# Kernel tuning notes

Hardware: AMD Instinct MI355X
Metric: run time of the kernel (lower is better)

Reference implementation:

```python
import jax, jax.numpy as jnp
import numpy as np

N, M, E, D = 20000, 1024, 640000, 256


def setup_inputs() -> dict:
    key = jax.random.key(0)
    ks = jax.random.split(key, 24)
    mask = jax.random.uniform(ks[0], (N, M)) < 0.05
    init = jnp.where(mask, jax.random.uniform(ks[1], (N, M), minval=0.1, maxval=1.0), 0.0)
    inp = {
        'init': init,
        'ei_cc': jax.random.randint(ks[2], (2, E), 0, N, dtype=jnp.int32),
        'ei_cac': jax.random.randint(ks[3], (2, E), 0, N, dtype=jnp.int32),
        'ei_csc': jax.random.randint(ks[4], (2, E), 0, N, dtype=jnp.int32),
        'ea_cc': jax.random.uniform(ks[5], (E,), minval=0.1, maxval=1.0),
        'ea_cac': jax.random.uniform(ks[6], (E,), minval=0.1, maxval=1.0),
        'ea_csc': jax.random.uniform(ks[7], (E,), minval=0.1, maxval=1.0),
        # Projection MLP: Linear(1,16) -> ReLU -> Linear(16,D)
        'pW1': jax.random.normal(ks[8], (1, 16)) * 0.5,
        'pb1': jnp.zeros((16,)),
        'pW2': jax.random.normal(ks[9], (16, D)) * 0.1,
        'pb2': jnp.zeros((D,)),
        # three GCN branches, 3 layers each (all D->D)
        'W_cc': jax.random.normal(ks[10], (3, D, D)) * 0.05,
        'b_cc': jnp.zeros((3, D)),
        'W_cac': jax.random.normal(ks[11], (3, D, D)) * 0.05,
        'b_cac': jnp.zeros((3, D)),
        'W_csc': jax.random.normal(ks[12], (3, D, D)) * 0.05,
        'b_csc': jnp.zeros((3, D)),
        # meta-path attention: Linear(D, 1)
        'w_att': jax.random.normal(ks[13], (D,)) * 0.05,
        'b_att': jnp.zeros((1,)),
    }
    return inp


def projection(init, pW1, pb1, pW2, pb2):
    # torch code feeds the *indices* of nonzero columns through the MLP and
    # mean-pools per row. Vectorize: precompute MLP(j) for every column index j,
    # then masked mean.
    idx = jnp.arange(M, dtype=init.dtype)[:, None]          # [M, 1]
    h = jax.nn.relu(idx @ pW1 + pb1)                        # [M, 16]
    col_emb = h @ pW2 + pb2                                 # [M, D]
    mask = (init != 0).astype(init.dtype)                   # [N, M]
    cnt = mask.sum(axis=1)                                  # [N]
    emb = (mask @ col_emb) / jnp.maximum(cnt, 1.0)[:, None]
    return jnp.where(cnt[:, None] > 0, emb, 0.0)            # zero rows stay zero


def gcn_conv(x, edge_index, edge_weight, W, b):
    # PyG GCNConv with edge_weight: add self loops (w=1), symmetric norm.
    n = x.shape[0]
    loop = jnp.arange(n, dtype=edge_index.dtype)
    row = jnp.concatenate([edge_index[0], loop])
    col = jnp.concatenate([edge_index[1], loop])
    w = jnp.concatenate([edge_weight, jnp.ones((n,), x.dtype)])
    deg = jax.ops.segment_sum(w, col, num_segments=n)
    dinv = jnp.where(deg > 0, jax.lax.rsqrt(deg), 0.0)
    norm = dinv[row] * w * dinv[col]                        # [E+N]
    h = x @ W                                               # [N, D]
    out = jax.ops.segment_sum(norm[:, None] * h[row], col, num_segments=n)
    return out + b


def gcn_branch(x, edge_index, edge_weight, Ws, bs):
    for l in range(3):
        x = jax.nn.relu(gcn_conv(x, edge_index, edge_weight, Ws[l], bs[l]))
    return x


def reference(init, ei_cc, ei_cac, ei_csc, ea_cc, ea_cac, ea_csc,
              pW1, pb1, pW2, pb2, W_cc, b_cc, W_cac, b_cac, W_csc, b_csc,
              w_att, b_att):
    x0 = projection(init, pW1, pb1, pW2, pb2)               # [N, D]
    out_cc = gcn_branch(x0, ei_cc, ea_cc, W_cc, b_cc)
    out_cac = gcn_branch(x0, ei_cac, ea_cac, W_cac, b_cac)
    out_csc = gcn_branch(x0, ei_csc, ea_csc, W_csc, b_csc)
    emb = jnp.stack([out_cc, out_cac, out_csc], axis=0)     # [3, N, D]
    scores = jnp.einsum('pnd,d->pn', emb, w_att) + b_att[0] # [3, N]
    attn = jax.nn.softmax(scores, axis=0)                   # softmax over meta-paths
    return jnp.einsum('pn,pnd->nd', attn, emb)              # [N, D]
```

## Files before the change

### kernel.cpp

```cpp
#include <hip/hip_runtime.h>
#include <hip/hip_bf16.h>

typedef __hip_bfloat16 bf16;
typedef __bf16 v8bf __attribute__((ext_vector_type(8)));
typedef float f32x4 __attribute__((ext_vector_type(4)));
typedef unsigned int v4u __attribute__((ext_vector_type(4)));

constexpr int N = 20000, M = 1024, E = 640000, D = 256;
constexpr size_t SEGEL = (size_t)N * D;
constexpr int NCHUNK = 10000;
constexpr int NSLICE = 64;
constexpr int ESLICE = E / NSLICE;

__device__ __forceinline__ float b2f(bf16 v) { return __bfloat162float(v); }
__device__ __forceinline__ bf16 f2b(float f) { return __float2bfloat16(f); }
__device__ __forceinline__ float u2f(unsigned short u) { return __uint_as_float(((unsigned)u) << 16); }
__device__ __forceinline__ unsigned short f2u(float f) { bf16 h = __float2bfloat16(f); return *(unsigned short*)&h; }
__device__ __forceinline__ float loadf(const void* p, size_t i, int isbf) {
    return isbf ? b2f(((const bf16*)p)[i]) : ((const float*)p)[i];
}
__device__ __forceinline__ void fma8(float* acc, uint4 v, float w) {
    acc[0] = fmaf(w, u2f((unsigned short)(v.x & 0xffffu)), acc[0]);
    acc[1] = fmaf(w, u2f((unsigned short)(v.x >> 16)), acc[1]);
    acc[2] = fmaf(w, u2f((unsigned short)(v.y & 0xffffu)), acc[2]);
    acc[3] = fmaf(w, u2f((unsigned short)(v.y >> 16)), acc[3]);
    acc[4] = fmaf(w, u2f((unsigned short)(v.z & 0xffffu)), acc[4]);
    acc[5] = fmaf(w, u2f((unsigned short)(v.z >> 16)), acc[5]);
    acc[6] = fmaf(w, u2f((unsigned short)(v.w & 0xffffu)), acc[6]);
    acc[7] = fmaf(w, u2f((unsigned short)(v.w >> 16)), acc[7]);
}
__device__ __forceinline__ void add8(float* a, uint4 v) {
    a[0] += u2f((unsigned short)(v.x & 0xffffu));
    a[1] += u2f((unsigned short)(v.x >> 16));
    a[2] += u2f((unsigned short)(v.y & 0xffffu));
    a[3] += u2f((unsigned short)(v.y >> 16));
    a[4] += u2f((unsigned short)(v.z & 0xffffu));
    a[5] += u2f((unsigned short)(v.z >> 16));
    a[6] += u2f((unsigned short)(v.w & 0xffffu));
    a[7] += u2f((unsigned short)(v.w >> 16));
}
__device__ __forceinline__ unsigned pack2(float a, float b) {
    return (unsigned)f2u(a) | ((unsigned)f2u(b) << 16);
}

__global__ void detect_kernel(const void* __restrict__ ea, int* __restrict__ flag)
{
    if (threadIdx.x == 0 && blockIdx.x == 0) {
        const unsigned short* u = (const unsigned short*)ea;
        int cnt = 0;
        for (int i = 0; i < 64; i++) {
            float f = __uint_as_float(((unsigned)u[i]) << 16);
            if (f >= 0.05f && f <= 1.05f) cnt++;
        }
        *flag = (cnt >= 60) ? 1 : 0;
    }
}

__global__ __launch_bounds__(256) void prep_kernel(
    const void* __restrict__ W0, const void* __restrict__ W1, const void* __restrict__ W2,
    const void* __restrict__ pW1, const void* __restrict__ pb1,
    const void* __restrict__ pW2, const void* __restrict__ pb2,
    bf16* __restrict__ WT, bf16* __restrict__ cemb, const int* __restrict__ flag)
{
    int isbf = *flag;
    int b = blockIdx.x;
    if (b < 2304) {
        int mat = b >> 8, n = b & 255, k = threadIdx.x;
        const void* W = (mat < 3) ? W0 : (mat < 6) ? W1 : W2;
        int lm = mat - (mat < 3 ? 0 : (mat < 6 ? 3 : 6));
        WT[(size_t)mat * 65536 + n * 256 + k] =
            f2b(loadf(W, (size_t)lm * 65536 + k * 256 + n, isbf));
    } else {
        int j = b - 2304;
        int d = threadIdx.x;
        float jf = (float)j;
        float acc = loadf(pb2, d, isbf);
        #pragma unroll
        for (int k = 0; k < 16; k++) {
            float h = fmaxf(jf * loadf(pW1, k, isbf) + loadf(pb1, k, isbf), 0.0f);
            acc += h * loadf(pW2, k * 256 + d, isbf);
        }
        cemb[(size_t)j * 256 + d] = f2b(acc);
    }
}

__global__ __launch_bounds__(256) void projection_kernel(
    const void* __restrict__ init, const bf16* __restrict__ cemb,
    bf16* __restrict__ x0, const int* __restrict__ flag)
{
    __shared__ unsigned short idxs[4][1024];
    int isbf = *flag;
    int wave = threadIdx.x >> 6, lane = threadIdx.x & 63;
    int i = blockIdx.x * 4 + wave;
    unsigned long long below = (lane == 63) ? 0x7fffffffffffffffull
                                            : ((1ull << lane) - 1ull);
    int cnt = 0;
    if (isbf) {
        const unsigned short* row = (const unsigned short*)init + (size_t)i * 1024;
        for (int c0 = 0; c0 < 1024; c0 += 64) {
            bool nz = (row[c0 + lane] & 0x7fffu) != 0;
            unsigned long long m = __ballot(nz);
            if (nz) idxs[wave][cnt + __popcll(m & below)] = (unsigned short)(c0 + lane);
            cnt += __popcll(m);
        }
    } else {
        const float* row = (const float*)init + (size_t)i * 1024;
        for (int c0 = 0; c0 < 1024; c0 += 64) {
            bool nz = row[c0 + lane] != 0.0f;
            unsigned long long m = __ballot(nz);
            if (nz) idxs[wave][cnt + __popcll(m & below)] = (unsigned short)(c0 + lane);
            cnt += __popcll(m);
        }
    }
    const uint4* cr4 = (const uint4*)cemb;
    int L = lane & 31, h = lane >> 5;
    float acc[8] = {0.f, 0.f, 0.f, 0.f, 0.f, 0.f, 0.f, 0.f};
    int npair = cnt >> 1;
    int t = 0;
    for (; t + 8 <= npair; t += 8) {
        uint4 v0 = cr4[(size_t)idxs[wave][2 * (t + 0) + h] * 32 + L];
        uint4 v1 = cr4[(size_t)idxs[wave][2 * (t + 1) + h] * 32 + L];
        uint4 v2 = cr4[(size_t)idxs[wave][2 * (t + 2) + h] * 32 + L];
        uint4 v3 = cr4[(size_t)idxs[wave][2 * (t + 3) + h] * 32 + L];
        uint4 v4 = cr4[(size_t)idxs[wave][2 * (t + 4) + h] * 32 + L];
        uint4 v5 = cr4[(size_t)idxs[wave][2 * (t + 5) + h] * 32 + L];
        uint4 v6 = cr4[(size_t)idxs[wave][2 * (t + 6) + h] * 32 + L];
        uint4 v7 = cr4[(size_t)idxs[wave][2 * (t + 7) + h] * 32 + L];
        add8(acc, v0); add8(acc, v1); add8(acc, v2); add8(acc, v3);
        add8(acc, v4); add8(acc, v5); add8(acc, v6); add8(acc, v7);
    }
    for (; t < npair; t++) {
        uint4 v = cr4[(size_t)idxs[wave][2 * t + h] * 32 + L];
        add8(acc, v);
    }
    if ((cnt & 1) && h == 0) {
        uint4 v = cr4[(size_t)idxs[wave][cnt - 1] * 32 + L];
        add8(acc, v);
    }
    #pragma unroll
    for (int j = 0; j < 8; j++) acc[j] += __shfl_xor(acc[j], 32, 64);
    if (h == 0) {
        float rinv = 1.0f / fmaxf((float)cnt, 1.0f);
        v4u o;
        o.x = pack2(acc[0] * rinv, acc[1] * rinv);
        o.y = pack2(acc[2] * rinv, acc[3] * rinv);
        o.z = pack2(acc[4] * rinv, acc[5] * rinv);
        o.w = pack2(acc[6] * rinv, acc[7] * rinv);
        ((v4u*)x0)[(size_t)i * 32 + L] = o;
    }
}

__global__ __launch_bounds__(256) void countP_kernel(
    const int* __restrict__ e0, const int* __restrict__ e1, const int* __restrict__ e2,
    int* __restrict__ P)
{
    __shared__ int cur[NCHUNK];
    int b = blockIdx.x;
    int pb = b >> 7, rem = b & 127;
    int ck = rem >> 6, s = rem & 63;
    const int* ei = pb == 0 ? e0 : pb == 1 ? e1 : e2;
    int c0 = ck * NCHUNK;
    int t = threadIdx.x;
    for (int i = t; i < NCHUNK; i += 256) cur[i] = 0;
    __syncthreads();
    int ebase = s * ESLICE;
    for (int e = ebase + t; e < ebase + ESLICE; e += 256) {
        int c = ei[E + e];
        if (c >= c0 && c < c0 + NCHUNK) atomicAdd(&cur[c - c0], 1);
    }
    __syncthreads();
    int* Prow = P + ((size_t)(pb * NSLICE + s)) * N + c0;
    for (int i = t; i < NCHUNK; i += 256) Prow[i] = cur[i];
}

__global__ __launch_bounds__(256) void cnt_sum_kernel(
    const int* __restrict__ P, int* __restrict__ cnt)
{
    int id = blockIdx.x * 256 + threadIdx.x;
    if (id >= 3 * N) return;
    int pb = id / N, c = id - pb * N;
    int sum = 0;
    #pragma unroll 8
    for (int s = 0; s < NSLICE; s++)
        sum += P[((size_t)(pb * NSLICE + s)) * N + c];
    cnt[id] = sum;
}

__global__ __launch_bounds__(1024) void scan_kernel(
    const int* __restrict__ cnt, int* __restrict__ col_ptr)
{
    int pb = blockIdx.x;
    int base = pb * E;
    __shared__ int s[1024];
    int t = threadIdx.x;
    const int CH = 20;
    int i0 = t * CH;
    int sum = 0;
    for (int j = 0; j < CH; j++) { int i = i0 + j; if (i < N) sum += cnt[pb * N + i]; }
    s[t] = sum;
    __syncthreads();
    for (int off = 1; off < 1024; off <<= 1) {
        int v = (t >= off) ? s[t - off] : 0;
        __syncthreads();
        s[t] += v;
        __syncthreads();
    }
    int run = base + s[t] - sum;
    for (int j = 0; j < CH; j++) {
        int i = i0 + j;
        if (i < N) {
            col_ptr[pb * (N + 1) + i] = run;
            run += cnt[pb * N + i];
        }
    }
    if (t == 0) col_ptr[pb * (N + 1) + N] = base + E;
}

__global__ __launch_bounds__(256) void base_kernel(
    int* __restrict__ P, const int* __restrict__ col_ptr)
{
    int id = blockIdx.x * 256 + threadIdx.x;
    if (id >= 3 * N) return;
    int pb = id / N, c = id - pb * N;
    int run = col_ptr[pb * (N + 1) + c];
    for (int s = 0; s < NSLICE; s++) {
        size_t idx = ((size_t)(pb * NSLICE + s)) * N + c;
        int v = P[idx];
        P[idx] = run;
        run += v;
    }
}

__global__ __launch_bounds__(256) void fill_kernel(
    const int* __restrict__ e0, const int* __restrict__ e1, const int* __restrict__ e2,
    const void* __restrict__ a0, const void* __restrict__ a1, const void* __restrict__ a2,
    const int* __restrict__ P, int2* __restrict__ epack, const int* __restrict__ flag)
{
    __shared__ int cur[NCHUNK];
    int isbf = *flag;
    int b = blockIdx.x;
    int pb = b >> 7, rem = b & 127;
    int ck = rem >> 6, s = rem & 63;
    const int* ei = pb == 0 ? e0 : pb == 1 ? e1 : e2;
    const void* ea = pb == 0 ? a0 : pb == 1 ? a1 : a2;
    int c0 = ck * NCHUNK;
    int t = threadIdx.x;
    const int* Prow = P + ((size_t)(pb * NSLICE + s)) * N + c0;
    for (int i = t; i < NCHUNK; i += 256) cur[i] = Prow[i];
    __syncthreads();
    int ebase = s * ESLICE;
    for (int e = ebase + t; e < ebase + ESLICE; e += 256) {
        int c = ei[E + e];
        if (c >= c0 && c < c0 + NCHUNK) {
            int r = ei[e];
            float w = loadf(ea, e, isbf);
            int pos = atomicAdd(&cur[c - c0], 1);
            int2 v; v.x = r; v.y = __float_as_int(w);
            epack[pos] = v;
        }
    }
}

__global__ __launch_bounds__(256) void degsum_kernel(
    const int* __restrict__ col_ptr, const int2* __restrict__ epack,
    float* __restrict__ dinv, float* __restrict__ nloop)
{
    int wave = threadIdx.x >> 6, lane = threadIdx.x & 63;
    int pb = blockIdx.x / 5000;
    int i = (blockIdx.x - pb * 5000) * 4 + wave;
    int start = col_ptr[pb * (N + 1) + i], end = col_ptr[pb * (N + 1) + i + 1];
    float sum = 0.0f;
    for (int p = start + lane; p < end; p += 64) sum += __int_as_float(epack[p].y);
    for (int off = 1; off < 64; off <<= 1) sum += __shfl_xor(sum, off, 64);
    if (lane == 0) {
        float dg = 1.0f + sum;
        dinv[pb * N + i] = rsqrtf(dg);
        nloop[pb * N + i] = 1.0f / dg;
    }
}

__global__ __launch_bounds__(256) void snorm_sort_kernel(
    const int* __restrict__ col_ptr, const int2* __restrict__ epack,
    unsigned* __restrict__ epk2, const float* __restrict__ dinv)
{
    int wave = threadIdx.x >> 6, lane = threadIdx.x & 63;
    int pb = blockIdx.x / 5000;
    int i = (blockIdx.x - pb * 5000) * 4 + wave;
    int start = col_ptr[pb * (N + 1) + i], end = col_ptr[pb * (N + 1) + i + 1];
    float dc = dinv[pb * N + i];
    for (int base = start; base < end; base += 64) {
        int n = end - base; n = n < 64 ? n : 64;
        int key = 0x7fffffff, val = 0;
        if (lane < n) {
            int2 v = epack[base + lane];
            key = v.x;
            val = __float_as_int(dc * __int_as_float(v.y) * dinv[pb * N + v.x]);
        }
        #pragma unroll
        for (int k = 2; k <= 64; k <<= 1) {
            #pragma unroll
            for (int j = k >> 1; j > 0; j >>= 1) {
                int pk = __shfl_xor(key, j, 64);
                int pv = __shfl_xor(val, j, 64);
                bool up = (lane & k) == 0;
                bool lower = (lane & j) == 0;
                bool takeMin = (up == lower);
                bool sw = takeMin ? (pk < key) : (pk > key);
                if (sw) { key = pk; val = pv; }
            }
        }
        if (lane < n) {
            epk2[base + lane] = (unsigned)key
                              | ((unsigned)f2u(__int_as_float(val)) << 16);
        }
    }
}

__global__ __launch_bounds__(256) void aggregate_kernel(
    const bf16* __restrict__ xi0, const bf16* __restrict__ xi1, const bf16* __restrict__ xi2,
    bf16* __restrict__ yb,
    const int* __restrict__ col_ptr, const unsigned* __restrict__ epk2,
    const float* __restrict__ nloop)
{
    int wave = threadIdx.x >> 6, lane = threadIdx.x & 63;
    int pb = blockIdx.x / 5000;
    int i = (blockIdx.x - pb * 5000) * 4 + wave;
    const bf16* x = pb == 0 ? xi0 : pb == 1 ? xi1 : xi2;
    const uint4* xr = (const uint4*)x;
    int L = lane & 31, h = lane >> 5;
    int start = col_ptr[pb * (N + 1) + i], end = col_ptr[pb * (N + 1) + i + 1];
    float nl = nloop[pb * N + i];
    float acc[8];
    {
        uint4 sv = xr[(size_t)i * 32 + L];
        float self = (h == 0) ? nl : 0.0f;
        #pragma unroll
        for (int j = 0; j < 8; j++) acc[j] = 0.0f;
        fma8(acc, sv, self);
    }
    for (int base = start; base < end; base += 64) {
        int n = end - base; n = n < 64 ? n : 64;
        int ev = 0;
        if (lane < n)
            ev = (int)__builtin_nontemporal_load(epk2 + base + lane);
        int pmax = (n + 1) >> 1;
        for (int p0 = 0; p0 < pmax; p0 += 8) {
            int m = pmax - p0; m = m < 8 ? m : 8;
            uint4 v[8];
            float w[8];
            #pragma unroll
            for (int k = 0; k < 8; k++) {
                int e = 2 * (p0 + k) + h;
                int ee = __shfl(ev, e, 64);
                int rj = ee & 0xffff;
                w[k] = u2f((unsigned short)((unsigned)ee >> 16));
                if (k < m) v[k] = xr[(size_t)rj * 32 + L];
            }
            #pragma unroll
            for (int k = 0; k < 8; k++)
                if (k < m) fma8(acc, v[k], w[k]);
        }
    }
    #pragma unroll
    for (int j = 0; j < 8; j++) acc[j] += __shfl_xor(acc[j], 32, 64);
    if (h == 0) {
        v4u o;
        o.x = pack2(acc[0], acc[1]);
        o.y = pack2(acc[2], acc[3]);
        o.z = pack2(acc[4], acc[5]);
        o.w = pack2(acc[6], acc[7]);
        __builtin_nontemporal_store(o,
            (v4u*)yb + (size_t)pb * (SEGEL / 8) + (size_t)i * 32 + L);
    }
}

__global__ __launch_bounds__(256) void gemm_relu_kernel(
    const bf16* __restrict__ yb, const bf16* __restrict__ WT, int layer,
    const void* __restrict__ b0, const void* __restrict__ b1, const void* __restrict__ b2,
    bf16* __restrict__ o0, bf16* __restrict__ o1, bf16* __restrict__ o2,
    const int* __restrict__ flag)
{
    constexpr int BPL = 157;
    int isbf = *flag;
    int pl = blockIdx.x / BPL, blk = blockIdx.x - pl * BPL;
    const bf16* y = yb + (size_t)pl * SEGEL;
    const bf16* wt = WT + (size_t)(pl * 3 + layer) * 65536;
    const void* bias = pl == 0 ? b0 : pl == 1 ? b1 : b2;
    bf16* xout = pl == 0 ? o0 : pl == 1 ? o1 : o2;

    int wave = threadIdx.x >> 6, lane = threadIdx.x & 63;
    int wr = wave >> 1, wn = wave & 1;
    int m0 = blk * 128 + wr * 64;
    int n0 = wn * 128;
    int mrow = lane & 15, q = lane >> 4;

    int ar[4];
    #pragma unroll
    for (int rs = 0; rs < 4; rs++) {
        int r = m0 + rs * 16 + mrow;
        ar[rs] = r < N ? r : N - 1;
    }

    f32x4 acc[4][8] = {};
    for (int k0 = 0; k0 < 256; k0 += 32) {
        int kq = (k0 >> 3) + q;
        v8bf b[8];
        #pragma unroll
        for (int nt = 0; nt < 8; nt++)
            b[nt] = reinterpret_cast<const v8bf*>(wt + (size_t)(n0 + nt * 16 + mrow) * 256)[kq];
        #pragma unroll
        for (int rs = 0; rs < 4; rs++) {
            v8bf a = reinterpret_cast<const v8bf*>(y + (size_t)ar[rs] * 256)[kq];
            #pragma unroll
            for (int nt = 0; nt < 8; nt++)
                acc[rs][nt] = __builtin_amdgcn_mfma_f32_16x16x32_bf16(a, b[nt], acc[rs][nt], 0, 0, 0);
        }
    }
    #pragma unroll
    for (int nt = 0; nt < 8; nt++) {
        int col = n0 + nt * 16 + mrow;
        float bv = loadf(bias, (size_t)layer * 256 + col, isbf);
        #pragma unroll
        for (int rs = 0; rs < 4; rs++) {
            #pragma unroll
            for (int r = 0; r < 4; r++) {
                int row = m0 + rs * 16 + q * 4 + r;
                if (row < N)
                    xout[(size_t)row * 256 + col] = f2b(fmaxf(acc[rs][nt][r] + bv, 0.0f));
            }
        }
    }
}

__global__ __launch_bounds__(256) void attention_kernel(
    const bf16* __restrict__ e0, const bf16* __restrict__ e1, const bf16* __restrict__ e2,
    const void* __restrict__ w_att, void* __restrict__ out, int n_nodes,
    const int* __restrict__ flag)
{
    int isbf = *flag;
    int wave = threadIdx.x >> 6, lane = threadIdx.x & 63;
    int n = blockIdx.x * 4 + wave;
    if (n >= n_nodes) return;
    int d0 = lane * 4;
    float w[4], v0[4], v1[4], v2[4];
    #pragma unroll
    for (int j = 0; j < 4; j++) {
        w[j]  = loadf(w_att, d0 + j, isbf);
        v0[j] = b2f(e0[(size_t)n * 256 + d0 + j]);
        v1[j] = b2f(e1[(size_t)n * 256 + d0 + j]);
        v2[j] = b2f(e2[(size_t)n * 256 + d0 + j]);
    }
    float s0 = 0, s1 = 0, s2 = 0;
    #pragma unroll
    for (int j = 0; j < 4; j++) { s0 += v0[j] * w[j]; s1 += v1[j] * w[j]; s2 += v2[j] * w[j]; }
    for (int off = 1; off < 64; off <<= 1) {
        s0 += __shfl_xor(s0, off, 64);
        s1 += __shfl_xor(s1, off, 64);
        s2 += __shfl_xor(s2, off, 64);
    }
    float m = fmaxf(s0, fmaxf(s1, s2));
    float a0 = expf(s0 - m), a1 = expf(s1 - m), a2 = expf(s2 - m);
    float inv = 1.0f / (a0 + a1 + a2);
    a0 *= inv; a1 *= inv; a2 *= inv;
    #pragma unroll
    for (int j = 0; j < 4; j++) {
        float v = a0 * v0[j] + a1 * v1[j] + a2 * v2[j];
        if (isbf) ((bf16*)out)[(size_t)n * 256 + d0 + j] = f2b(v);
        else      ((float*)out)[(size_t)n * 256 + d0 + j] = v;
    }
}

extern "C" void kernel_launch(void* const* d_in, const int* in_sizes, int n_in,
                              void* d_out, int out_size, void* d_ws, size_t ws_size,
                              hipStream_t stream)
{
    (void)in_sizes; (void)n_in; (void)out_size; (void)ws_size;

    const void* init = d_in[0];
    const int*  ei[3] = {(const int*)d_in[1], (const int*)d_in[2], (const int*)d_in[3]};
    const void* ea[3] = {d_in[4], d_in[5], d_in[6]};
    const void* pW1 = d_in[7];
    const void* pb1 = d_in[8];
    const void* pW2 = d_in[9];
    const void* pb2 = d_in[10];
    const void* Wb[3] = {d_in[11], d_in[13], d_in[15]};
    const void* bb[3] = {d_in[12], d_in[14], d_in[16]};
    const void* w_att = d_in[17];

    char* ws = (char*)d_ws;
    size_t off = 0;
    auto carve = [&](size_t bytes) -> char* {
        off = (off + 255) & ~(size_t)255;
        char* p = ws + off; off += bytes; return p;
    };
    int*   flag  = (int*)carve(4);
    bf16*  WT    = (bf16*)carve((size_t)9 * 65536 * 2);
    bf16*  cemb  = (bf16*)carve((size_t)M * D * 2);
    bf16*  x0    = (bf16*)carve(SEGEL * 2);
    int*   cnt   = (int*)carve((size_t)3 * N * 4);
    int*   colp  = (int*)carve((size_t)3 * (N + 1) * 4);
    float* dinv  = (float*)carve((size_t)3 * N * 4);
    float* nloop = (float*)carve((size_t)3 * N * 4);
    int2*  epack = (int2*)carve((size_t)3 * E * 8);
    unsigned* epk2 = (unsigned*)carve((size_t)3 * E * 4);
    bf16*  ybuf  = (bf16*)carve((size_t)3 * SEGEL * 2);
    bf16*  bufA  = (bf16*)carve((size_t)3 * SEGEL * 2);
    bf16*  bufB  = (bf16*)carve((size_t)3 * SEGEL * 2);
    int* P = (int*)bufB;

    detect_kernel<<<1, 64, 0, stream>>>(ea[0], flag);
    prep_kernel<<<3328, 256, 0, stream>>>(Wb[0], Wb[1], Wb[2],
                                          pW1, pb1, pW2, pb2, WT, cemb, flag);
    projection_kernel<<<5000, 256, 0, stream>>>(init, cemb, x0, flag);

    countP_kernel<<<384, 256, 0, stream>>>(ei[0], ei[1], ei[2], P);
    cnt_sum_kernel<<<(3 * N + 255) / 256, 256, 0, stream>>>(P, cnt);
    scan_kernel<<<3, 1024, 0, stream>>>(cnt, colp);
    base_kernel<<<(3 * N + 255) / 256, 256, 0, stream>>>(P, colp);
    fill_kernel<<<384, 256, 0, stream>>>(ei[0], ei[1], ei[2], ea[0], ea[1], ea[2],
                                         P, epack, flag);
    degsum_kernel<<<15000, 256, 0, stream>>>(colp, epack, dinv, nloop);
    snorm_sort_kernel<<<15000, 256, 0, stream>>>(colp, epack, epk2, dinv);

    const bf16 *i0 = x0, *i1 = x0, *i2 = x0;
    bf16* dsts[3] = {bufA, bufB, bufA};
    for (int l = 0; l < 3; l++) {
        aggregate_kernel<<<15000, 256, 0, stream>>>(i0, i1, i2, ybuf, colp, epk2, nloop);
        bf16* dst = dsts[l];
        gemm_relu_kernel<<<3 * 157, 256, 0, stream>>>(ybuf, WT, l, bb[0], bb[1], bb[2],
                                                      dst, dst + SEGEL, dst + 2 * SEGEL, flag);
        i0 = dst; i1 = dst + SEGEL; i2 = dst + 2 * SEGEL;
    }
    attention_kernel<<<5000, 256, 0, stream>>>(bufA, bufA + SEGEL, bufA + 2 * SEGEL,
                                               w_att, d_out, N, flag);
}
```

Baseline: 871.1 us.

## Inline dtype detection per kernel and shrink GEMM tiles to 32 rows

Drops the single-thread detect kernel and its flag buffer; each kernel now works out the bf16/f32 input format itself with a wave ballot over the first 64 edge weights. The GEMM is retiled from 128-row blocks with a 4x8 MFMA accumulator per wave to 32-row blocks with one 16-row strip per wave, which raises the block count from 471 to 1875. The aim is to remove one launch plus the serial detection, and to improve occupancy and fill more CUs in the GEMM. In exchange each loaded B fragment is reused less, the row bounds guard is removed (20000 divides evenly by 32), and every thread repeats a small global read for detection.

Result: no change. 885.7 us (+1.7%).

```diff
diff --git a/kernel.cpp b/kernel.cpp
--- a/kernel.cpp
+++ b/kernel.cpp
@@ -18,6 +18,12 @@
 __device__ __forceinline__ unsigned short f2u(float f) { bf16 h = __float2bfloat16(f); return *(unsigned short*)&h; }
 __device__ __forceinline__ float loadf(const void* p, size_t i, int isbf) {
     return isbf ? b2f(((const bf16*)p)[i]) : ((const float*)p)[i];
+}
+__device__ __forceinline__ int detect_bf(const void* ea) {
+    int lane = threadIdx.x & 63;
+    float f = u2f(((const unsigned short*)ea)[lane]);
+    bool ok = (f >= 0.05f && f <= 1.05f);
+    return __popcll(__ballot(ok)) >= 60;
 }
 __device__ __forceinline__ void fma8(float* acc, uint4 v, float w) {
     acc[0] = fmaf(w, u2f((unsigned short)(v.x & 0xffffu)), acc[0]);
@@ -43,26 +49,13 @@
     return (unsigned)f2u(a) | ((unsigned)f2u(b) << 16);
 }
 
-__global__ void detect_kernel(const void* __restrict__ ea, int* __restrict__ flag)
-{
-    if (threadIdx.x == 0 && blockIdx.x == 0) {
-        const unsigned short* u = (const unsigned short*)ea;
-        int cnt = 0;
-        for (int i = 0; i < 64; i++) {
-            float f = __uint_as_float(((unsigned)u[i]) << 16);
-            if (f >= 0.05f && f <= 1.05f) cnt++;
-        }
-        *flag = (cnt >= 60) ? 1 : 0;
-    }
-}
-
 __global__ __launch_bounds__(256) void prep_kernel(
     const void* __restrict__ W0, const void* __restrict__ W1, const void* __restrict__ W2,
     const void* __restrict__ pW1, const void* __restrict__ pb1,
     const void* __restrict__ pW2, const void* __restrict__ pb2,
-    bf16* __restrict__ WT, bf16* __restrict__ cemb, const int* __restrict__ flag)
-{
-    int isbf = *flag;
+    bf16* __restrict__ WT, bf16* __restrict__ cemb, const void* __restrict__ ea0)
+{
+    int isbf = detect_bf(ea0);
     int b = blockIdx.x;
     if (b < 2304) {
         int mat = b >> 8, n = b & 255, k = threadIdx.x;
@@ -86,10 +79,10 @@
 
 __global__ __launch_bounds__(256) void projection_kernel(
     const void* __restrict__ init, const bf16* __restrict__ cemb,
-    bf16* __restrict__ x0, const int* __restrict__ flag)
+    bf16* __restrict__ x0, const void* __restrict__ ea0)
 {
     __shared__ unsigned short idxs[4][1024];
-    int isbf = *flag;
+    int isbf = detect_bf(ea0);
     int wave = threadIdx.x >> 6, lane = threadIdx.x & 63;
     int i = blockIdx.x * 4 + wave;
     unsigned long long below = (lane == 63) ? 0x7fffffffffffffffull
@@ -234,10 +227,10 @@
 __global__ __launch_bounds__(256) void fill_kernel(
     const int* __restrict__ e0, const int* __restrict__ e1, const int* __restrict__ e2,
     const void* __restrict__ a0, const void* __restrict__ a1, const void* __restrict__ a2,
-    const int* __restrict__ P, int2* __restrict__ epack, const int* __restrict__ flag)
+    const int* __restrict__ P, int2* __restrict__ epack)
 {
     __shared__ int cur[NCHUNK];
-    int isbf = *flag;
+    int isbf = detect_bf(a0);
     int b = blockIdx.x;
     int pb = b >> 7, rem = b & 127;
     int ck = rem >> 6, s = rem & 63;
@@ -378,42 +371,28 @@
     const bf16* __restrict__ yb, const bf16* __restrict__ WT, int layer,
     const void* __restrict__ b0, const void* __restrict__ b1, const void* __restrict__ b2,
     bf16* __restrict__ o0, bf16* __restrict__ o1, bf16* __restrict__ o2,
-    const int* __restrict__ flag)
-{
-    constexpr int BPL = 157;
-    int isbf = *flag;
-    int pl = blockIdx.x / BPL, blk = blockIdx.x - pl * BPL;
+    const void* __restrict__ ea0)
+{
+    int isbf = detect_bf(ea0);
+    int pl = blockIdx.x / 625, blk = blockIdx.x - pl * 625;
     const bf16* y = yb + (size_t)pl * SEGEL;
     const bf16* wt = WT + (size_t)(pl * 3 + layer) * 65536;
     const void* bias = pl == 0 ? b0 : pl == 1 ? b1 : b2;
     bf16* xout = pl == 0 ? o0 : pl == 1 ? o1 : o2;
 
     int wave = threadIdx.x >> 6, lane = threadIdx.x & 63;
-    int wr = wave >> 1, wn = wave & 1;
-    int m0 = blk * 128 + wr * 64;
-    int n0 = wn * 128;
+    int m0 = blk * 32 + (wave >> 1) * 16;
+    int n0 = (wave & 1) * 128;
     int mrow = lane & 15, q = lane >> 4;
 
-    int ar[4];
-    #pragma unroll
-    for (int rs = 0; rs < 4; rs++) {
-        int r = m0 + rs * 16 + mrow;
-        ar[rs] = r < N ? r : N - 1;
-    }
-
-    f32x4 acc[4][8] = {};
+    f32x4 acc[8] = {};
+    const v8bf* arow = reinterpret_cast<const v8bf*>(y + (size_t)(m0 + mrow) * 256);
     for (int k0 = 0; k0 < 256; k0 += 32) {
-        int kq = (k0 >> 3) + q;
-        v8bf b[8];
+        v8bf a = arow[(k0 >> 3) + q];
         #pragma unroll
-        for (int nt = 0; nt < 8; nt++)
-            b[nt] = reinterpret_cast<const v8bf*>(wt + (size_t)(n0 + nt * 16 + mrow) * 256)[kq];
-        #pragma unroll
-        for (int rs = 0; rs < 4; rs++) {
-            v8bf a = reinterpret_cast<const v8bf*>(y + (size_t)ar[rs] * 256)[kq];
-            #pragma unroll
-            for (int nt = 0; nt < 8; nt++)
-                acc[rs][nt] = __builtin_amdgcn_mfma_f32_16x16x32_bf16(a, b[nt], acc[rs][nt], 0, 0, 0);
+        for (int nt = 0; nt < 8; nt++) {
+            const v8bf* brow = reinterpret_cast<const v8bf*>(wt + (size_t)(n0 + nt * 16 + mrow) * 256);
+            acc[nt] = __builtin_amdgcn_mfma_f32_16x16x32_bf16(a, brow[(k0 >> 3) + q], acc[nt], 0, 0, 0);
         }
     }
     #pragma unroll
@@ -421,13 +400,9 @@
         int col = n0 + nt * 16 + mrow;
         float bv = loadf(bias, (size_t)layer * 256 + col, isbf);
         #pragma unroll
-        for (int rs = 0; rs < 4; rs++) {
-            #pragma unroll
-            for (int r = 0; r < 4; r++) {
-                int row = m0 + rs * 16 + q * 4 + r;
-                if (row < N)
-                    xout[(size_t)row * 256 + col] = f2b(fmaxf(acc[rs][nt][r] + bv, 0.0f));
-            }
+        for (int r = 0; r < 4; r++) {
+            int row = m0 + q * 4 + r;
+            xout[(size_t)row * 256 + col] = f2b(fmaxf(acc[nt][r] + bv, 0.0f));
         }
     }
 }
@@ -435,9 +410,9 @@
 __global__ __launch_bounds__(256) void attention_kernel(
     const bf16* __restrict__ e0, const bf16* __restrict__ e1, const bf16* __restrict__ e2,
     const void* __restrict__ w_att, void* __restrict__ out, int n_nodes,
-    const int* __restrict__ flag)
-{
-    int isbf = *flag;
+    const void* __restrict__ ea0)
+{
+    int isbf = detect_bf(ea0);
     int wave = threadIdx.x >> 6, lane = threadIdx.x & 63;
     int n = blockIdx.x * 4 + wave;
     if (n >= n_nodes) return;
@@ -493,7 +468,6 @@
         off = (off + 255) & ~(size_t)255;
         char* p = ws + off; off += bytes; return p;
     };
-    int*   flag  = (int*)carve(4);
     bf16*  WT    = (bf16*)carve((size_t)9 * 65536 * 2);
     bf16*  cemb  = (bf16*)carve((size_t)M * D * 2);
     bf16*  x0    = (bf16*)carve(SEGEL * 2);
@@ -508,17 +482,16 @@
     bf16*  bufB  = (bf16*)carve((size_t)3 * SEGEL * 2);
     int* P = (int*)bufB;
 
-    detect_kernel<<<1, 64, 0, stream>>>(ea[0], flag);
     prep_kernel<<<3328, 256, 0, stream>>>(Wb[0], Wb[1], Wb[2],
-                                          pW1, pb1, pW2, pb2, WT, cemb, flag);
-    projection_kernel<<<5000, 256, 0, stream>>>(init, cemb, x0, flag);
+                                          pW1, pb1, pW2, pb2, WT, cemb, ea[0]);
+    projection_kernel<<<5000, 256, 0, stream>>>(init, cemb, x0, ea[0]);
 
     countP_kernel<<<384, 256, 0, stream>>>(ei[0], ei[1], ei[2], P);
     cnt_sum_kernel<<<(3 * N + 255) / 256, 256, 0, stream>>>(P, cnt);
     scan_kernel<<<3, 1024, 0, stream>>>(cnt, colp);
     base_kernel<<<(3 * N + 255) / 256, 256, 0, stream>>>(P, colp);
     fill_kernel<<<384, 256, 0, stream>>>(ei[0], ei[1], ei[2], ea[0], ea[1], ea[2],
-                                         P, epack, flag);
+                                         P, epack);
     degsum_kernel<<<15000, 256, 0, stream>>>(colp, epack, dinv, nloop);
     snorm_sort_kernel<<<15000, 256, 0, stream>>>(colp, epack, epk2, dinv);
 
@@ -527,10 +500,10 @@
     for (int l = 0; l < 3; l++) {
         aggregate_kernel<<<15000, 256, 0, stream>>>(i0, i1, i2, ybuf, colp, epk2, nloop);
         bf16* dst = dsts[l];
-        gemm_relu_kernel<<<3 * 157, 256, 0, stream>>>(ybuf, WT, l, bb[0], bb[1], bb[2],
-                                                      dst, dst + SEGEL, dst + 2 * SEGEL, flag);
+        gemm_relu_kernel<<<1875, 256, 0, stream>>>(ybuf, WT, l, bb[0], bb[1], bb[2],
+                                                   dst, dst + SEGEL, dst + 2 * SEGEL, ea[0]);
         i0 = dst; i1 = dst + SEGEL; i2 = dst + 2 * SEGEL;
     }
     attention_kernel<<<5000, 256, 0, stream>>>(bufA, bufA + SEGEL, bufA + 2 * SEGEL,
-                                               w_att, d_out, N, flag);
-}
+                                               w_att, d_out, N, ea[0]);
+}
```
